# Kernel optimization log

Hardware: AMD Instinct MI355X
Metric: run time of the kernel (lower is better)

The kernel has to match this reference:

```python
import jax, jax.numpy as jnp
import numpy as np

B, N, D = 2, 256, 256

def setup_inputs() -> dict:
    key = jax.random.key(0)
    ks = jax.random.split(key, 8)
    s = 1.0 / np.sqrt(D)
    return {
        "node_features": jax.random.normal(ks[0], (B, N, D), jnp.float32),
        "edge_features": jax.random.normal(ks[1], (B, N, N, D), jnp.float32),
        "adj_matrix": jax.random.randint(ks[2], (B, N, N), 0, 2, jnp.int32),
        "WA": jax.random.normal(ks[3], (D, D), jnp.float32) * s,
        "bA": jnp.zeros((D,), jnp.float32),
        "WB": jax.random.normal(ks[4], (D, D), jnp.float32) * s,
        "bB": jnp.zeros((D,), jnp.float32),
        "WC": jax.random.normal(ks[5], (D, D), jnp.float32) * s,
        "bC": jnp.zeros((D,), jnp.float32),
        "WU": jax.random.normal(ks[6], (D, D), jnp.float32) * s,
        "bU": jnp.zeros((D,), jnp.float32),
        "WV": jax.random.normal(ks[7], (D, D), jnp.float32) * s,
        "bV": jnp.zeros((D,), jnp.float32),
    }

def reference(node_features, edge_features, adj_matrix,
              WA, bA, WB, bB, WC, bC, WU, bU, WV, bV):
    h, e = node_features, edge_features
    Ah = h @ WA + bA                      # [B,N,D]
    Bh = h @ WB + bB                      # [B,N,D]
    Ce = jnp.einsum('bijd,de->bije', e, WC) + bC  # [B,N,N,D]
    # edge update: broadcast sum, relu, residual (normalization='none')
    e_new = Ah[:, None, :, :] + Bh[:, :, None, :] + Ce
    e_out = e + jax.nn.relu(e_new)        # [B,N,N,D]
    edge_gates = jax.nn.sigmoid(e_out)    # [B,N,N,D]
    Uh = h @ WU + bU                      # [B,N,D]
    Vh = h @ WV + bV                      # [B,N,D]
    # aggregate: gated sum over axis=2 (neighbor j), mean by row degree
    msgs = jnp.einsum('bijd,bjd->bid', edge_gates, Vh)  # sum_j gates*Vh
    deg = jnp.sum(adj_matrix, axis=-1, keepdims=True).astype(Vh.dtype)  # [B,N,1]
    agg = msgs / deg
    h_out = h + jax.nn.relu(Uh + agg)     # [B,N,D]
    return h_out, e_out
```

## Files before the change

### kernel.cpp

```cpp
#include <hip/hip_runtime.h>
#include <cstdint>
#include <cstddef>


#define AH_OFF 0
#define BH_OFF 131072
#define UH_OFF 262144
#define VH_OFF 393216
#define MS_OFF 524288
#define WC_BYTE_OFF 2621440

typedef __attribute__((ext_vector_type(4))) float vfloat4;
typedef __attribute__((ext_vector_type(4))) short vshort4;
typedef __attribute__((ext_vector_type(8))) short vshort8;

__device__ inline unsigned short bf16_rne(float x) {
    unsigned u = __builtin_bit_cast(unsigned, x);
    u += 0x7fffu + ((u >> 16) & 1u);
    return (unsigned short)(u >> 16);
}

__device__ inline void gload_lds16(const void* g, void* l) {
    __builtin_amdgcn_global_load_lds(
        (const __attribute__((address_space(1))) void*)g,
        (__attribute__((address_space(3))) void*)l, 16, 0, 0);
}

__device__ inline vfloat4 mfma_16x16x32_bf16(vshort8 a, vshort8 b, vfloat4 c) {
    asm("v_mfma_f32_16x16x32_bf16 %0, %1, %2, %0" : "+v"(c) : "v"(a), "v"(b));
    return c;
}

__global__ void __launch_bounds__(256)
ggcn_prep(const float* __restrict__ h,
          const float* __restrict__ WA, const float* __restrict__ bA,
          const float* __restrict__ WB, const float* __restrict__ bB,
          const float* __restrict__ WC,
          const float* __restrict__ WU, const float* __restrict__ bU,
          const float* __restrict__ WV, const float* __restrict__ bV,
          float* __restrict__ ws) {
    int bid = blockIdx.x, tid = threadIdx.x;
    if (bid < 128) {
        __shared__ float hs[4][256];
        int gm0 = bid * 4;
        vfloat4 hv = *(const vfloat4*)(h + gm0 * 256 + tid * 4);
        ((vfloat4*)(&hs[0][0]))[tid] = hv;
        __syncthreads();
        float aA[4] = {0, 0, 0, 0}, aB[4] = {0, 0, 0, 0};
        float aU[4] = {0, 0, 0, 0}, aV[4] = {0, 0, 0, 0};
        int d = tid;
        for (int k = 0; k < 256; ++k) {
            float wa = WA[k * 256 + d], wb = WB[k * 256 + d];
            float wu = WU[k * 256 + d], wv = WV[k * 256 + d];
#pragma unroll
            for (int mm = 0; mm < 4; ++mm) {
                float hh = hs[mm][k];
                aA[mm] = fmaf(hh, wa, aA[mm]);
                aB[mm] = fmaf(hh, wb, aB[mm]);
                aU[mm] = fmaf(hh, wu, aU[mm]);
                aV[mm] = fmaf(hh, wv, aV[mm]);
            }
        }
        float ba = bA[d], bb = bB[d], bu = bU[d], bv = bV[d];
#pragma unroll
        for (int mm = 0; mm < 4; ++mm) {
            int o = (gm0 + mm) * 256 + d;
            ws[AH_OFF + o] = aA[mm] + ba;
            ws[BH_OFF + o] = aB[mm] + bb;
            ws[UH_OFF + o] = aU[mm] + bu;
            ws[VH_OFF + o] = aV[mm] + bv;
        }
    } else if (bid < 192) {
        unsigned short* wc = (unsigned short*)((char*)ws + WC_BYTE_OFF);
        int local = bid - 128;
#pragma unroll
        for (int r = 0; r < 4; ++r) {
            int idx = local * 1024 + r * 256 + tid;
            int slab = idx >> 13;
            int rem = idx & 8191;
            int kg = rem >> 11;
            int d = (rem >> 3) & 255;
            int e = rem & 7;
            int k = slab * 32 + kg * 8 + e;
            wc[idx] = bf16_rne(WC[k * 256 + d]);
        }
    } else {
        int local = bid - 192;
#pragma unroll
        for (int r = 0; r < 8; ++r)
            ws[MS_OFF + local * 2048 + r * 256 + tid] = 0.f;
    }
}

__global__ void __launch_bounds__(256, 2)
ggcn_main(const float* __restrict__ eg,
          const float* __restrict__ bC,
          float* __restrict__ ws,
          float* __restrict__ out) {
    extern __shared__ char smem[];
    int tid = threadIdx.x;
    int lane = tid & 63, wid = tid >> 6;
    int bidx = blockIdx.x;
    int m = bidx >> 3;
    int jt0 = (bidx & 7) * 32;
    int bb = m >> 8;
    size_t ebase0 = (size_t)m * 65536 + (size_t)jt0 * 256;

#pragma unroll
    for (int r = 0; r < 8; ++r) {
        vfloat4 v = *(const vfloat4*)(eg + ebase0 + r * 1024 + tid * 4);
        int j = r * 4 + wid;
        int kg = lane >> 1;
        int off = kg * 512 + (((j ^ kg) << 4) | ((lane & 1) * 8));
        vshort4 hi, lo;
#pragma unroll
        for (int t = 0; t < 4; ++t) {
            unsigned short h16 = bf16_rne(v[t]);
            float hf = __builtin_bit_cast(float, (unsigned)h16 << 16);
            hi[t] = (short)h16;
            lo[t] = (short)bf16_rne(v[t] - hf);
        }
        *(vshort4*)(smem + off) = hi;
        *(vshort4*)(smem + 16384 + off) = lo;
    }

    const char* wcb = (const char*)ws + WC_BYTE_OFF;
    auto loadB = [&](int s, int buf) {
        const char* src = wcb + s * 16384;
        char* dst = smem + 32768 + buf * 16384;
#pragma unroll
        for (int r = 0; r < 4; ++r) {
            int off = (wid * 4 + r) * 1024;
            gload_lds16(src + off + lane * 16, dst + off);
        }
    };
    loadB(0, 0);
    __syncthreads();

    int col = lane & 15, rgrp = lane >> 4;
    int wd0 = wid * 64;

    vfloat4 acc[2][4];
#pragma unroll
    for (int jf = 0; jf < 2; ++jf)
#pragma unroll
        for (int df = 0; df < 4; ++df) acc[jf][df] = (vfloat4){0.f, 0.f, 0.f, 0.f};

    for (int s = 0; s < 8; ++s) {
        int cur = s & 1;
        if (s < 7) loadB(s + 1, cur ^ 1);
        const char* bbuf = smem + 32768 + cur * 16384;
        int kgA = s * 4 + rgrp;
        vshort8 ah[2], al[2], bv[4];
#pragma unroll
        for (int jf = 0; jf < 2; ++jf) {
            int ab = kgA * 512 + (((jf * 16 + col) ^ kgA) << 4);
            ah[jf] = *(const vshort8*)(smem + ab);
            al[jf] = *(const vshort8*)(smem + 16384 + ab);
        }
#pragma unroll
        for (int df = 0; df < 4; ++df)
            bv[df] = *(const vshort8*)(bbuf + rgrp * 4096 + (wd0 + df * 16 + col) * 16);
#pragma unroll
        for (int jf = 0; jf < 2; ++jf)
#pragma unroll
            for (int df = 0; df < 4; ++df) {
                acc[jf][df] = mfma_16x16x32_bf16(ah[jf], bv[df], acc[jf][df]);
                acc[jf][df] = mfma_16x16x32_bf16(al[jf], bv[df], acc[jf][df]);
            }
        __syncthreads();
    }

    float bc[4], bh[4];
#pragma unroll
    for (int df = 0; df < 4; ++df) {
        int d = wd0 + df * 16 + col;
        bc[df] = bC[d];
        bh[df] = ws[BH_OFF + m * 256 + d];
    }
    float macc[4] = {0, 0, 0, 0};
    float* eo_out = out + 131072;
#pragma unroll
    for (int jf = 0; jf < 2; ++jf) {
#pragma unroll
        for (int r = 0; r < 4; ++r) {
            int jg = jt0 + jf * 16 + rgrp * 4 + r;
            size_t rowoff = (size_t)(bb * 256 + jg) * 256;
            size_t erow = (size_t)m * 65536 + (size_t)jg * 256;
#pragma unroll
            for (int df = 0; df < 4; ++df) {
                int d = wd0 + df * 16 + col;
                float ce = acc[jf][df][r] + bc[df];
                float en = ws[AH_OFF + rowoff + d] + bh[df] + ce;
                float eo = eg[erow + d] + fmaxf(en, 0.f);
                eo_out[erow + d] = eo;
                float g = __builtin_amdgcn_rcpf(1.f + __expf(-eo));
                macc[df] = fmaf(g, ws[VH_OFF + rowoff + d], macc[df]);
            }
        }
    }
#pragma unroll
    for (int df = 0; df < 4; ++df) {
        float v = macc[df];
        v += __shfl_xor(v, 16, 64);
        v += __shfl_xor(v, 32, 64);
        if (lane < 16)
            atomicAdd(&ws[MS_OFF + m * 256 + wd0 + df * 16 + col], v);
    }
}

__global__ void __launch_bounds__(256)
ggcn_final(const float* __restrict__ h, const int* __restrict__ adj,
           const float* __restrict__ ws, float* __restrict__ out) {
    __shared__ float parts[4];
    int m = blockIdx.x, tid = threadIdx.x;
    float v = (float)adj[m * 256 + tid];
#pragma unroll
    for (int o = 1; o < 64; o <<= 1) v += __shfl_xor(v, o, 64);
    if ((tid & 63) == 0) parts[tid >> 6] = v;
    __syncthreads();
    float deg = parts[0] + parts[1] + parts[2] + parts[3];
    int o = m * 256 + tid;
    out[o] = h[o] + fmaxf(0.f, ws[UH_OFF + o] + ws[MS_OFF + o] / deg);
}

extern "C" void kernel_launch(void* const* d_in, const int* in_sizes, int n_in,
                              void* d_out, int out_size, void* d_ws, size_t ws_size,
                              hipStream_t stream) {
    const float* h   = (const float*)d_in[0];
    const float* eg  = (const float*)d_in[1];
    const int*   adj = (const int*)d_in[2];
    const float* WA  = (const float*)d_in[3];
    const float* bA  = (const float*)d_in[4];
    const float* WB  = (const float*)d_in[5];
    const float* bB  = (const float*)d_in[6];
    const float* WC  = (const float*)d_in[7];
    const float* bC  = (const float*)d_in[8];
    const float* WU  = (const float*)d_in[9];
    const float* bU  = (const float*)d_in[10];
    const float* WV  = (const float*)d_in[11];
    const float* bV  = (const float*)d_in[12];
    float* out = (float*)d_out;
    float* ws  = (float*)d_ws;

    ggcn_prep<<<256, 256, 0, stream>>>(h, WA, bA, WB, bB, WC, WU, bU, WV, bV, ws);
    ggcn_main<<<4096, 256, 65536, stream>>>(eg, bC, ws, out);
    ggcn_final<<<512, 256, 0, stream>>>(h, adj, ws, out);
}
```

Measured before the change: 333.9 us.

## Use MFMA for node projections and reuse LDS edge tile in epilogue

Rewrites the node projection prep kernel to use split-bf16 MFMA with LDS-staged inputs and weights instead of scalar FMA loops. The main kernel moves to 512-thread blocks with one j-half per wave, raising wave count per block. The epilogue reconstructs the edge value from the hi/lo bf16 copy already in LDS instead of re-reading it from global memory, cutting global traffic at a small precision cost.

```diff
diff --git a/kernel.cpp b/kernel.cpp
--- a/kernel.cpp
+++ b/kernel.cpp
@@ -18,6 +18,10 @@
     unsigned u = __builtin_bit_cast(unsigned, x);
     u += 0x7fffu + ((u >> 16) & 1u);
     return (unsigned short)(u >> 16);
+}
+
+__device__ inline float bf16_to_f(unsigned short h) {
+    return __builtin_bit_cast(float, (unsigned)h << 16);
 }
 
 __device__ inline void gload_lds16(const void* g, void* l) {
@@ -39,60 +43,117 @@
           const float* __restrict__ WU, const float* __restrict__ bU,
           const float* __restrict__ WV, const float* __restrict__ bV,
           float* __restrict__ ws) {
+    extern __shared__ char smem[];
     int bid = blockIdx.x, tid = threadIdx.x;
-    if (bid < 128) {
-        __shared__ float hs[4][256];
-        int gm0 = bid * 4;
-        vfloat4 hv = *(const vfloat4*)(h + gm0 * 256 + tid * 4);
-        ((vfloat4*)(&hs[0][0]))[tid] = hv;
+
+    if (bid < 256) {
+        int rt = bid & 15;
+        int ct = bid >> 4;
+        int mat = ct >> 2;
+        const float* Wm = (mat == 0) ? WA : (mat == 1) ? WB : (mat == 2) ? WU : WV;
+        int cm0 = (ct & 3) * 64;
+
+#pragma unroll
+        for (int r = 0; r < 8; ++r) {
+            int flat = r * 1024 + tid * 4;
+            int row_l = flat >> 8, k = flat & 255;
+            vfloat4 v = *(const vfloat4*)(h + (rt * 32 + row_l) * 256 + k);
+            int kg = k >> 3;
+            int off = kg * 512 + (((row_l ^ kg) << 4) | ((k & 7) * 2));
+            vshort4 hi, lo;
+#pragma unroll
+            for (int t = 0; t < 4; ++t) {
+                unsigned short h16 = bf16_rne(v[t]);
+                hi[t] = (short)h16;
+                lo[t] = (short)bf16_rne(v[t] - bf16_to_f(h16));
+            }
+            *(vshort4*)(smem + off) = hi;
+            *(vshort4*)(smem + 16384 + off) = lo;
+        }
+
+        auto stageW = [&](int s, int buf) {
+            char* base = smem + 32768 + buf * 16384;
+#pragma unroll
+            for (int rr = 0; rr < 4; ++rr) {
+                int k_l = rr * 16 + (tid >> 4);
+                int c_l = (tid & 15) * 4;
+                vfloat4 v = *(const vfloat4*)(Wm + (s * 64 + k_l) * 256 + cm0 + c_l);
+                int boff = (k_l >> 3) * 1024 + (k_l & 7) * 2;
+#pragma unroll
+                for (int t = 0; t < 4; ++t) {
+                    unsigned short h16 = bf16_rne(v[t]);
+                    unsigned short l16 = bf16_rne(v[t] - bf16_to_f(h16));
+                    *(unsigned short*)(base + boff + (c_l + t) * 16) = h16;
+                    *(unsigned short*)(base + 8192 + boff + (c_l + t) * 16) = l16;
+                }
+            }
+        };
+        stageW(0, 0);
         __syncthreads();
-        float aA[4] = {0, 0, 0, 0}, aB[4] = {0, 0, 0, 0};
-        float aU[4] = {0, 0, 0, 0}, aV[4] = {0, 0, 0, 0};
-        int d = tid;
-        for (int k = 0; k < 256; ++k) {
-            float wa = WA[k * 256 + d], wb = WB[k * 256 + d];
-            float wu = WU[k * 256 + d], wv = WV[k * 256 + d];
-#pragma unroll
-            for (int mm = 0; mm < 4; ++mm) {
-                float hh = hs[mm][k];
-                aA[mm] = fmaf(hh, wa, aA[mm]);
-                aB[mm] = fmaf(hh, wb, aB[mm]);
-                aU[mm] = fmaf(hh, wu, aU[mm]);
-                aV[mm] = fmaf(hh, wv, aV[mm]);
+
+        int lane = tid & 63, w = tid >> 6;
+        int col = lane & 15, rgrp = lane >> 4;
+        int c_lane = w * 16 + col;
+
+        vfloat4 acc[2];
+        acc[0] = (vfloat4){0.f, 0.f, 0.f, 0.f};
+        acc[1] = (vfloat4){0.f, 0.f, 0.f, 0.f};
+
+        for (int s = 0; s < 4; ++s) {
+            if (s < 3) stageW(s + 1, (s + 1) & 1);
+            const char* bbuf = smem + 32768 + (s & 1) * 16384;
+#pragma unroll
+            for (int step = 0; step < 2; ++step) {
+                int kgB = step * 4 + rgrp;
+                vshort8 bhi = *(const vshort8*)(bbuf + kgB * 1024 + c_lane * 16);
+                vshort8 blo = *(const vshort8*)(bbuf + 8192 + kgB * 1024 + c_lane * 16);
+                int kgA = s * 8 + kgB;
+#pragma unroll
+                for (int mf = 0; mf < 2; ++mf) {
+                    int ab = kgA * 512 + (((mf * 16 + col) ^ kgA) << 4);
+                    vshort8 ahi = *(const vshort8*)(smem + ab);
+                    vshort8 alo = *(const vshort8*)(smem + 16384 + ab);
+                    acc[mf] = mfma_16x16x32_bf16(ahi, bhi, acc[mf]);
+                    acc[mf] = mfma_16x16x32_bf16(alo, bhi, acc[mf]);
+                    acc[mf] = mfma_16x16x32_bf16(ahi, blo, acc[mf]);
+                }
             }
-        }
-        float ba = bA[d], bb = bB[d], bu = bU[d], bv = bV[d];
-#pragma unroll
-        for (int mm = 0; mm < 4; ++mm) {
-            int o = (gm0 + mm) * 256 + d;
-            ws[AH_OFF + o] = aA[mm] + ba;
-            ws[BH_OFF + o] = aB[mm] + bb;
-            ws[UH_OFF + o] = aU[mm] + bu;
-            ws[VH_OFF + o] = aV[mm] + bv;
-        }
-    } else if (bid < 192) {
+            __syncthreads();
+        }
+
+        const float* bp = (mat == 0) ? bA : (mat == 1) ? bB : (mat == 2) ? bU : bV;
+        int cm = cm0 + c_lane;
+        float bias = bp[cm];
+        float* ob = ws + (mat == 0 ? AH_OFF : mat == 1 ? BH_OFF : mat == 2 ? UH_OFF : VH_OFF);
+#pragma unroll
+        for (int mf = 0; mf < 2; ++mf)
+#pragma unroll
+            for (int rr = 0; rr < 4; ++rr) {
+                int row = rt * 32 + mf * 16 + rgrp * 4 + rr;
+                ob[row * 256 + cm] = acc[mf][rr] + bias;
+            }
+    } else if (bid < 320) {
         unsigned short* wc = (unsigned short*)((char*)ws + WC_BYTE_OFF);
-        int local = bid - 128;
+        int local = bid - 256;
 #pragma unroll
         for (int r = 0; r < 4; ++r) {
             int idx = local * 1024 + r * 256 + tid;
             int slab = idx >> 13;
-            int rem = idx & 8191;
-            int kg = rem >> 11;
-            int d = (rem >> 3) & 255;
-            int e = rem & 7;
+            int kg = (idx >> 11) & 3;
+            int d = (idx >> 3) & 255;
+            int e = idx & 7;
             int k = slab * 32 + kg * 8 + e;
             wc[idx] = bf16_rne(WC[k * 256 + d]);
         }
     } else {
-        int local = bid - 192;
+        int local = bid - 320;
 #pragma unroll
         for (int r = 0; r < 8; ++r)
             ws[MS_OFF + local * 2048 + r * 256 + tid] = 0.f;
     }
 }
 
-__global__ void __launch_bounds__(256, 2)
+__global__ void __launch_bounds__(512, 4)
 ggcn_main(const float* __restrict__ eg,
           const float* __restrict__ bC,
           float* __restrict__ ws,
@@ -107,18 +168,19 @@
     size_t ebase0 = (size_t)m * 65536 + (size_t)jt0 * 256;
 
 #pragma unroll
-    for (int r = 0; r < 8; ++r) {
-        vfloat4 v = *(const vfloat4*)(eg + ebase0 + r * 1024 + tid * 4);
-        int j = r * 4 + wid;
-        int kg = lane >> 1;
-        int off = kg * 512 + (((j ^ kg) << 4) | ((lane & 1) * 8));
+    for (int r = 0; r < 4; ++r) {
+        int flat = r * 2048 + tid * 4;
+        vfloat4 v = *(const vfloat4*)(eg + ebase0 + flat);
+        int j = flat >> 8;
+        int k = flat & 255;
+        int kg = k >> 3;
+        int off = kg * 512 + (((j ^ kg) << 4) | ((k & 7) * 2));
         vshort4 hi, lo;
 #pragma unroll
         for (int t = 0; t < 4; ++t) {
             unsigned short h16 = bf16_rne(v[t]);
-            float hf = __builtin_bit_cast(float, (unsigned)h16 << 16);
             hi[t] = (short)h16;
-            lo[t] = (short)bf16_rne(v[t] - hf);
+            lo[t] = (short)bf16_rne(v[t] - bf16_to_f(h16));
         }
         *(vshort4*)(smem + off) = hi;
         *(vshort4*)(smem + 16384 + off) = lo;
@@ -129,74 +191,70 @@
         const char* src = wcb + s * 16384;
         char* dst = smem + 32768 + buf * 16384;
 #pragma unroll
-        for (int r = 0; r < 4; ++r) {
-            int off = (wid * 4 + r) * 1024;
-            gload_lds16(src + off + lane * 16, dst + off);
+        for (int rr = 0; rr < 2; ++rr) {
+            int off_u = (rr * 8 + wid) * 1024;
+            gload_lds16(src + off_u + lane * 16, dst + off_u);
         }
     };
     loadB(0, 0);
     __syncthreads();
 
     int col = lane & 15, rgrp = lane >> 4;
-    int wd0 = wid * 64;
-
-    vfloat4 acc[2][4];
-#pragma unroll
-    for (int jf = 0; jf < 2; ++jf)
-#pragma unroll
-        for (int df = 0; df < 4; ++df) acc[jf][df] = (vfloat4){0.f, 0.f, 0.f, 0.f};
+    int jh = wid >> 2, dq = wid & 3;
+    int d0 = dq * 64;
+
+    vfloat4 acc[4];
+#pragma unroll
+    for (int df = 0; df < 4; ++df) acc[df] = (vfloat4){0.f, 0.f, 0.f, 0.f};
 
     for (int s = 0; s < 8; ++s) {
         int cur = s & 1;
         if (s < 7) loadB(s + 1, cur ^ 1);
         const char* bbuf = smem + 32768 + cur * 16384;
         int kgA = s * 4 + rgrp;
-        vshort8 ah[2], al[2], bv[4];
-#pragma unroll
-        for (int jf = 0; jf < 2; ++jf) {
-            int ab = kgA * 512 + (((jf * 16 + col) ^ kgA) << 4);
-            ah[jf] = *(const vshort8*)(smem + ab);
-            al[jf] = *(const vshort8*)(smem + 16384 + ab);
-        }
+        int ab = kgA * 512 + (((jh * 16 + col) ^ kgA) << 4);
+        vshort8 ah = *(const vshort8*)(smem + ab);
+        vshort8 al = *(const vshort8*)(smem + 16384 + ab);
+        vshort8 bv[4];
 #pragma unroll
         for (int df = 0; df < 4; ++df)
-            bv[df] = *(const vshort8*)(bbuf + rgrp * 4096 + (wd0 + df * 16 + col) * 16);
-#pragma unroll
-        for (int jf = 0; jf < 2; ++jf)
-#pragma unroll
-            for (int df = 0; df < 4; ++df) {
-                acc[jf][df] = mfma_16x16x32_bf16(ah[jf], bv[df], acc[jf][df]);
-                acc[jf][df] = mfma_16x16x32_bf16(al[jf], bv[df], acc[jf][df]);
-            }
+            bv[df] = *(const vshort8*)(bbuf + rgrp * 4096 + (d0 + df * 16 + col) * 16);
+#pragma unroll
+        for (int df = 0; df < 4; ++df) {
+            acc[df] = mfma_16x16x32_bf16(ah, bv[df], acc[df]);
+            acc[df] = mfma_16x16x32_bf16(al, bv[df], acc[df]);
+        }
         __syncthreads();
     }
 
     float bc[4], bh[4];
 #pragma unroll
     for (int df = 0; df < 4; ++df) {
-        int d = wd0 + df * 16 + col;
+        int d = d0 + df * 16 + col;
         bc[df] = bC[d];
         bh[df] = ws[BH_OFF + m * 256 + d];
     }
     float macc[4] = {0, 0, 0, 0};
     float* eo_out = out + 131072;
 #pragma unroll
-    for (int jf = 0; jf < 2; ++jf) {
-#pragma unroll
-        for (int r = 0; r < 4; ++r) {
-            int jg = jt0 + jf * 16 + rgrp * 4 + r;
-            size_t rowoff = (size_t)(bb * 256 + jg) * 256;
-            size_t erow = (size_t)m * 65536 + (size_t)jg * 256;
-#pragma unroll
-            for (int df = 0; df < 4; ++df) {
-                int d = wd0 + df * 16 + col;
-                float ce = acc[jf][df][r] + bc[df];
-                float en = ws[AH_OFF + rowoff + d] + bh[df] + ce;
-                float eo = eg[erow + d] + fmaxf(en, 0.f);
-                eo_out[erow + d] = eo;
-                float g = __builtin_amdgcn_rcpf(1.f + __expf(-eo));
-                macc[df] = fmaf(g, ws[VH_OFF + rowoff + d], macc[df]);
-            }
+    for (int r = 0; r < 4; ++r) {
+        int jl = jh * 16 + rgrp * 4 + r;
+        int jg = jt0 + jl;
+        size_t rowoff = (size_t)(bb * 256 + jg) * 256;
+        size_t erow = (size_t)m * 65536 + (size_t)jg * 256;
+#pragma unroll
+        for (int df = 0; df < 4; ++df) {
+            int d = d0 + df * 16 + col;
+            int kg = d >> 3;
+            int aoff = kg * 512 + (((jl ^ kg) << 4) | ((d & 7) * 2));
+            float ev = bf16_to_f(*(const unsigned short*)(smem + aoff)) +
+                       bf16_to_f(*(const unsigned short*)(smem + 16384 + aoff));
+            float ce = acc[df][r] + bc[df];
+            float en = ws[AH_OFF + rowoff + d] + bh[df] + ce;
+            float eo = ev + fmaxf(en, 0.f);
+            eo_out[erow + d] = eo;
+            float g = __builtin_amdgcn_rcpf(1.f + __expf(-eo));
+            macc[df] = fmaf(g, ws[VH_OFF + rowoff + d], macc[df]);
         }
     }
 #pragma unroll
@@ -205,7 +263,7 @@
         v += __shfl_xor(v, 16, 64);
         v += __shfl_xor(v, 32, 64);
         if (lane < 16)
-            atomicAdd(&ws[MS_OFF + m * 256 + wd0 + df * 16 + col], v);
+            atomicAdd(&ws[MS_OFF + m * 256 + d0 + df * 16 + col], v);
     }
 }
 
@@ -243,7 +301,7 @@
     float* out = (float*)d_out;
     float* ws  = (float*)d_ws;
 
-    ggcn_prep<<<256, 256, 0, stream>>>(h, WA, bA, WB, bB, WC, WU, bU, WV, bV, ws);
-    ggcn_main<<<4096, 256, 65536, stream>>>(eg, bC, ws, out);
+    ggcn_prep<<<384, 256, 65536, stream>>>(h, WA, bA, WB, bB, WC, WU, bU, WV, bV, ws);
+    ggcn_main<<<4096, 512, 65536, stream>>>(eg, bC, ws, out);
     ggcn_final<<<512, 256, 0, stream>>>(h, adj, ws, out);
 }
```

New measurement: 292.4 us. 1.14x faster.
